# Kernel optimization log

Measured on AMD Instinct MI355X. Metric: run time of the kernel, lower is better.

Reference implementation:

```python
import jax, jax.numpy as jnp
import numpy as np

F_MAX = 16  # static max number of frames (torch code uses max(frames) dynamically)
B, C, H, W = 8, 5, 512, 512


def setup_inputs() -> dict:
    key = jax.random.key(0)
    k1, k2 = jax.random.split(key)
    inp = jax.random.normal(k1, (B, C, H, W), dtype=jnp.float32)
    frames = jax.random.randint(k2, (B,), 1, F_MAX + 1)  # n_frames per sample in [1, F_MAX]
    return {"input": inp, "frames": frames}


def _acquire(inp, frames, noise_key):
    b, _, h, w = inp.shape
    ku, kn = jax.random.split(noise_key)
    img = inp[:, :1]                                                   # [B,1,H,W]
    bias = jax.nn.relu(jnp.mean(inp[:, 1:2], axis=(1, 2, 3), keepdims=True))  # [B,1,1,1]
    sampled = img + bias                                               # broadcasts to [B,F_MAX,H,W] below
    center = img + bias                                                # [B,1,H,W]
    # Frechet noise
    fw = jax.nn.relu(inp[:, 2:3])                                      # weight [B,1,H,W]
    fa = jax.nn.relu(inp[:, 3:4])                                      # alpha  [B,1,H,W]
    u = jnp.clip(jax.random.uniform(ku, (b, F_MAX, h, w), dtype=inp.dtype), 1e-6, 1.0 - 1e-6)
    sampled = sampled + fw * (-jnp.log(u)) ** (-fa)                    # [B,F_MAX,H,W]
    center = center + fw * (1.0 / (fa + 1.0)) ** fa
    # Gaussian noise
    gw = jax.nn.relu(inp[:, 4:5])
    sampled = sampled + gw * jax.random.normal(kn, (b, F_MAX, h, w), dtype=inp.dtype)
    acquired_frames = jnp.clip(sampled, 0.0, 1.0)                      # [B,F_MAX,H,W]
    # ragged per-sample mean over first n_frames frames, vectorized via mask
    mask = (jnp.arange(F_MAX)[None, :, None, None] < frames[:, None, None, None]).astype(inp.dtype)
    frames_f = frames.astype(inp.dtype)[:, None, None, None]
    acquired = jnp.sum(acquired_frames * mask, axis=1, keepdims=True) / frames_f  # [B,1,H,W]
    return acquired, jnp.clip(center, 0.0, 1.0)


def reference(input, frames):
    return _acquire(input, frames, jax.random.key(42))
```

## Files before the change

kernel.cpp:

```cpp
#include <hip/hip_runtime.h>
#include <stdint.h>

#define HW 262144
#define ACQ_N 2097152
#define SREG 69632
#define NREG3 208896

#define CNT(b, c) ((((b) << 2) | (c)) << 5)

#define LOG2F(x) __builtin_amdgcn_logf(x)
#define EXP2F(x) __builtin_amdgcn_exp2f(x)
#define SQRTF(x) __builtin_amdgcn_sqrtf(x)
#define RCPF(x)  __builtin_amdgcn_rcpf(x)

#define ROTL(x, r) __builtin_amdgcn_alignbit((x), (x), (32 - (r)) & 31)

static inline void tf2x32_host(uint32_t k0, uint32_t k1, uint32_t c0, uint32_t c1,
                               uint32_t& o0, uint32_t& o1) {
  const uint32_t ks2 = k0 ^ k1 ^ 0x1BD11BDAu;
  uint32_t x0 = c0 + k0, x1 = c1 + k1;
#define TFR(r) { x0 += x1; x1 = (x1 << (r)) | (x1 >> (32 - (r))); x1 ^= x0; }
  TFR(13) TFR(15) TFR(26) TFR(6)
  x0 += k1;  x1 += ks2 + 1u;
  TFR(17) TFR(29) TFR(16) TFR(24)
  x0 += ks2; x1 += k0 + 2u;
  TFR(13) TFR(15) TFR(26) TFR(6)
  x0 += k0;  x1 += k1 + 3u;
  TFR(17) TFR(29) TFR(16) TFR(24)
  x0 += k1;  x1 += ks2 + 4u;
  TFR(13) TFR(15) TFR(26) TFR(6)
  x0 += ks2; x1 += k0 + 5u;
#undef TFR
  o0 = x0; o1 = x1;
}

__device__ __forceinline__ uint32_t rbits32(uint32_t k0, uint32_t k1, uint32_t idx) {
  const uint32_t ks2 = k0 ^ k1 ^ 0x1BD11BDAu;
  uint32_t x0 = k0, x1 = idx + k1;
#define TFR(r) { x0 += x1; x1 = ROTL(x1, r); x1 ^= x0; }
  TFR(13) TFR(15) TFR(26) TFR(6)
  x0 += k1;  x1 += ks2 + 1u;
  TFR(17) TFR(29) TFR(16) TFR(24)
  x0 += ks2; x1 += k0 + 2u;
  TFR(13) TFR(15) TFR(26) TFR(6)
  x0 += k0;  x1 += k1 + 3u;
  TFR(17) TFR(29) TFR(16) TFR(24)
  x0 += k1;  x1 += ks2 + 4u;
  TFR(13) TFR(15) TFR(26) TFR(6)
  x0 += ks2; x1 += k0 + 5u;
#undef TFR
  return x0 ^ x1;
}

__device__ __forceinline__ float unit_from_bits(uint32_t b) {
  return __uint_as_float((b >> 9) | 0x3F800000u) - 1.0f;
}

__device__ __forceinline__ float sqrt2_erfinv(float x) {
  float ome = fmaf(-x, x, 1.0f);
  float w = -0.69314718056f * LOG2F(ome);
  float wn = w - 2.5f;
  float p = 3.974065e-08f;
  p = fmaf(p, wn, 4.854641e-07f);
  p = fmaf(p, wn, -4.982823e-06f);
  p = fmaf(p, wn, -6.210531e-06f);
  p = fmaf(p, wn, 3.091200e-04f);
  p = fmaf(p, wn, -1.773035e-03f);
  p = fmaf(p, wn, -5.908135e-03f);
  p = fmaf(p, wn, 3.488029e-01f);
  p = fmaf(p, wn, 2.123314e+00f);
  if (__builtin_expect(w >= 5.0f, 0)) {
    float wf = SQRTF(w) - 3.0f;
    float q = -2.831458e-04f;
    q = fmaf(q, wf, 1.427657e-04f);
    q = fmaf(q, wf, 1.908260e-03f);
    q = fmaf(q, wf, -5.195013e-03f);
    q = fmaf(q, wf, 8.116892e-03f);
    q = fmaf(q, wf, -1.0779791e-02f);
    q = fmaf(q, wf, 1.3348579e-02f);
    q = fmaf(q, wf, 1.416582e+00f);
    q = fmaf(q, wf, 4.006434e+00f);
    p = q;
  }
  return p * x;
}

__device__ __forceinline__ float loop_fg(float base, float fw, float fa, float gw,
                                         uint32_t idx, int nf,
                                         uint32_t ku0, uint32_t ku1,
                                         uint32_t kn0, uint32_t kn1) {
  float nfa = -fa, fac = fa * 0.52876637294f;
  float acc = 0.0f;
#pragma unroll 2
  for (int f = 0; f < nf; ++f) {
    uint32_t ub = rbits32(ku0, ku1, idx);
    uint32_t nb = rbits32(kn0, kn1, idx);
    idx += (uint32_t)HW;
    float u = fminf(fmaxf(unit_from_bits(ub), 1e-6f), 0.999999f);
    float pw = EXP2F(fmaf(nfa, LOG2F(-LOG2F(u)), fac));
    float z = sqrt2_erfinv(fmaf(unit_from_bits(nb), 2.0f, -0.99999994f));
    float t = fmaf(gw, z, fmaf(fw, pw, base));
    acc += fminf(fmaxf(t, 0.0f), 1.0f);
  }
  return acc * RCPF((float)nf);
}

__device__ __forceinline__ float loop_f(float base, float fw, float fa,
                                        uint32_t idx, int nf,
                                        uint32_t ku0, uint32_t ku1) {
  float nfa = -fa, fac = fa * 0.52876637294f;
  float acc = 0.0f;
#pragma unroll 4
  for (int f = 0; f < nf; ++f) {
    uint32_t ub = rbits32(ku0, ku1, idx);
    idx += (uint32_t)HW;
    float u = fminf(fmaxf(unit_from_bits(ub), 1e-6f), 0.999999f);
    float pw = EXP2F(fmaf(nfa, LOG2F(-LOG2F(u)), fac));
    acc += fminf(fmaxf(fmaf(fw, pw, base), 0.0f), 1.0f);
  }
  return acc * RCPF((float)nf);
}

__device__ __forceinline__ float loop_g(float base, float gw,
                                        uint32_t idx, int nf,
                                        uint32_t kn0, uint32_t kn1) {
  float acc = 0.0f;
#pragma unroll 4
  for (int f = 0; f < nf; ++f) {
    uint32_t nb = rbits32(kn0, kn1, idx);
    idx += (uint32_t)HW;
    float z = sqrt2_erfinv(fmaf(unit_from_bits(nb), 2.0f, -0.99999994f));
    acc += fminf(fmaxf(fmaf(gw, z, base), 0.0f), 1.0f);
  }
  return acc * RCPF((float)nf);
}


__global__ __launch_bounds__(256) void bias_partial(const float* __restrict__ inp,
                                                    float* __restrict__ partial,
                                                    uint32_t* __restrict__ counters) {
  if (blockIdx.x == 0) {
    counters[threadIdx.x] = 0u;
    counters[256 + threadIdx.x] = 0u;
    counters[512 + threadIdx.x] = 0u;
    counters[768 + threadIdx.x] = 0u;
  }
  int blk = blockIdx.x;
  int b = blk >> 6, chunk = blk & 63;
  const float4* src = (const float4*)(inp + ((size_t)b * 5 + 1) * HW
                                          + (size_t)chunk * 4096);
  int t = threadIdx.x;
  float s = 0.0f;
#pragma unroll
  for (int k = 0; k < 4; ++k) {
    float4 v = src[t + k * 256];
    s += (v.x + v.y) + (v.z + v.w);
  }
  for (int off = 32; off; off >>= 1) s += __shfl_down(s, off);
  __shared__ float ws4[4];
  if ((t & 63) == 0) ws4[t >> 6] = s;
  __syncthreads();
  if (t == 0) partial[blk] = ws4[0] + ws4[1] + ws4[2] + ws4[3];
}

__global__ __launch_bounds__(256) void scatter_pack(const float* __restrict__ inp,
                                                    const float* __restrict__ partial,
                                                    uint32_t* __restrict__ counters,
                                                    uint32_t* __restrict__ remarr,
                                                    float4* __restrict__ packed,
                                                    float* __restrict__ out) {
  int blk = blockIdx.x;
  int b = blk >> 8, sub = blk & 255;
  int tid = threadIdx.x, lane = tid & 63, wid = tid >> 6;
  const float* pb = inp + (size_t)b * 5 * HW;
  uint64_t below = (1ull << lane) - 1ull;
  int base_i = sub << 10;

  __shared__ float s_bias;
  __shared__ uint32_t swcnt[4][4];
  __shared__ uint32_t sbase[4];

  if (tid < 64) {
    float s = partial[(b << 6) | tid];
    for (int o = 32; o; o >>= 1) s += __shfl_down(s, o);
    if (tid == 0) s_bias = fmaxf(s * (1.0f / 262144.0f), 0.0f);
  }

  float img4[4], fw4[4], fa4[4], gw4[4];
  uint32_t cls4[4];
  uint32_t wc1 = 0, wc2 = 0, wc3 = 0;
#pragma unroll
  for (int k = 0; k < 4; ++k) {
    int i = base_i + (k << 8) + tid;
    img4[k]  = pb[i];
    float f2 = pb[2 * HW + i];
    float f3 = pb[3 * HW + i];
    float f4 = pb[4 * HW + i];
    fw4[k] = fmaxf(f2, 0.0f);
    fa4[k] = fmaxf(f3, 0.0f);
    gw4[k] = fmaxf(f4, 0.0f);
    uint32_t cls = (f2 > 0.0f ? 1u : 0u) | (f4 > 0.0f ? 2u : 0u);
    cls4[k] = cls;
    wc1 += (uint32_t)__popcll(__ballot(cls == 1u));
    wc2 += (uint32_t)__popcll(__ballot(cls == 2u));
    wc3 += (uint32_t)__popcll(__ballot(cls == 3u));
  }
  if (lane == 0) {
    swcnt[wid][1] = wc1; swcnt[wid][2] = wc2; swcnt[wid][3] = wc3;
  }
  __syncthreads();
  if (tid < 3) {
    int c = tid + 1;
    uint32_t tot = swcnt[0][c] + swcnt[1][c] + swcnt[2][c] + swcnt[3][c];
    sbase[c] = atomicAdd(&counters[CNT(b, c)], tot);
  }
  __syncthreads();

  uint32_t run1 = sbase[1], run2 = sbase[2], run3 = sbase[3];
#pragma unroll
  for (int w = 0; w < 4; ++w) {
    if (w < wid) { run1 += swcnt[w][1]; run2 += swcnt[w][2]; run3 += swcnt[w][3]; }
  }
  float bias = s_bias;

  uint32_t* rbase = remarr + (size_t)b * NREG3;
  float4*   kbase = packed + (size_t)b * NREG3;
  float*    outa  = out + (size_t)b * HW;
  float*    outc  = out + ACQ_N + (size_t)b * HW;

#pragma unroll
  for (int k = 0; k < 4; ++k) {
    int i = base_i + (k << 8) + tid;
    float fw = fw4[k], fa = fa4[k], gw = gw4[k];
    float basev = img4[k] + bias;
    float cpw = EXP2F(-fa * LOG2F(fa + 1.0f));
    float ctr = fminf(fmaxf(fmaf(fw, cpw, basev), 0.0f), 1.0f);
    outc[i] = ctr;

    uint32_t cls = cls4[k];
    if (cls == 0u) outa[i] = ctr;

    uint64_t ba1 = __ballot(cls == 1u);
    uint64_t ba2 = __ballot(cls == 2u);
    uint64_t ba3 = __ballot(cls == 3u);
    if (cls != 0u) {
      uint64_t own  = (cls == 1u) ? ba1 : ((cls == 2u) ? ba2 : ba3);
      uint32_t rbas = (cls == 1u) ? run1 : ((cls == 2u) ? run2 : run3);
      uint32_t roff = (cls - 1u) * (uint32_t)SREG + rbas + (uint32_t)__popcll(own & below);
      rbase[roff] = (uint32_t)i;
      kbase[roff] = make_float4(basev, fw, fa, gw);
    }
    run1 += (uint32_t)__popcll(ba1);
    run2 += (uint32_t)__popcll(ba2);
    run3 += (uint32_t)__popcll(ba3);
  }
}

__global__ __launch_bounds__(256) void acquire_packed(
    const int* __restrict__ frames, const uint32_t* __restrict__ counters,
    const uint32_t* __restrict__ remarr, const float4* __restrict__ packed,
    float* __restrict__ out,
    uint32_t ku0, uint32_t ku1, uint32_t kn0, uint32_t kn1) {
  int c = 3 - (int)blockIdx.y;
  int b = (int)blockIdx.z;
  uint32_t cnt = counters[CNT(b, c)];
  uint32_t slot = ((uint32_t)blockIdx.x << 8) | (uint32_t)threadIdx.x;
  if (((uint32_t)blockIdx.x << 8) >= cnt) return;
  if (slot < cnt) {
    size_t roff = (size_t)b * NREG3 + (size_t)(c - 1) * SREG + slot;
    float4 op = packed[roff];
    uint32_t rem = remarr[roff];
    float base = op.x, fw = op.y, fa = op.z, gw = op.w;
    int nf = frames[b];
    uint32_t idx = ((uint32_t)b << 22) + rem;
    float res;
    if (c == 3)      res = loop_fg(base, fw, fa, gw, idx, nf, ku0, ku1, kn0, kn1);
    else if (c == 1) res = loop_f(base, fw, fa, idx, nf, ku0, ku1);
    else             res = loop_g(base, gw, idx, nf, kn0, kn1);
    out[(size_t)b * HW + rem] = res;
  }
}

__global__ __launch_bounds__(256) void bias_partial_plain(const float* __restrict__ inp,
                                                          float* __restrict__ partial) {
  int blk = blockIdx.x;
  int b = blk >> 6, chunk = blk & 63;
  const float4* src = (const float4*)(inp + ((size_t)b * 5 + 1) * HW
                                          + (size_t)chunk * 4096);
  int t = threadIdx.x;
  float s = 0.0f;
#pragma unroll
  for (int k = 0; k < 4; ++k) {
    float4 v = src[t + k * 256];
    s += (v.x + v.y) + (v.z + v.w);
  }
  for (int off = 32; off; off >>= 1) s += __shfl_down(s, off);
  __shared__ float ws4[4];
  if ((t & 63) == 0) ws4[t >> 6] = s;
  __syncthreads();
  if (t == 0) partial[blk] = ws4[0] + ws4[1] + ws4[2] + ws4[3];
}

__global__ __launch_bounds__(256) void acquire_plain(
    const float* __restrict__ inp, const int* __restrict__ frames,
    const float* __restrict__ partial, float* __restrict__ out,
    uint32_t ku0, uint32_t ku1, uint32_t kn0, uint32_t kn1) {
  int b = blockIdx.x >> 10;
  int rem = ((blockIdx.x & 1023) << 8) | threadIdx.x;
  __shared__ float s_bias;
  if (threadIdx.x < 64) {
    float s = partial[(b << 6) | threadIdx.x];
    for (int off = 32; off; off >>= 1) s += __shfl_down(s, off);
    if (threadIdx.x == 0) s_bias = fmaxf(s * (1.0f / 262144.0f), 0.0f);
  }
  const float* pb = inp + (size_t)b * 5 * HW;
  float img = pb[rem];
  float fw  = fmaxf(pb[2 * HW + rem], 0.0f);
  float fa  = fmaxf(pb[3 * HW + rem], 0.0f);
  float gw  = fmaxf(pb[4 * HW + rem], 0.0f);
  __syncthreads();
  float base = img + s_bias;
  int nf = frames[b];
  uint32_t idx = ((uint32_t)b << 22) + (uint32_t)rem;
  float res = loop_fg(base, fw, fa, gw, idx, nf, ku0, ku1, kn0, kn1);
  out[(size_t)b * HW + rem] = res;
  float cpw = EXP2F(-fa * LOG2F(fa + 1.0f));
  out[ACQ_N + (size_t)b * HW + rem] = fminf(fmaxf(fmaf(fw, cpw, base), 0.0f), 1.0f);
}

extern "C" void kernel_launch(void* const* d_in, const int* in_sizes, int n_in,
                              void* d_out, int out_size, void* d_ws, size_t ws_size,
                              hipStream_t stream) {
  const float* inp    = (const float*)d_in[0];
  const int*   frames = (const int*)d_in[1];
  float* out = (float*)d_out;

  uint32_t ku0, ku1, kn0, kn1;
  tf2x32_host(0u, 42u, 0u, 0u, ku0, ku1);
  tf2x32_host(0u, 42u, 0u, 1u, kn0, kn1);

  float*    partial  = (float*)d_ws;
  uint32_t* counters = (uint32_t*)((char*)d_ws + 4096);
  const size_t need_full = 8192 + (size_t)8 * NREG3 * 4 + (size_t)8 * NREG3 * 16;

  if (ws_size >= need_full) {
    uint32_t* remarr = (uint32_t*)((char*)d_ws + 8192);
    float4*   packed = (float4*)((char*)d_ws + 8192 + (size_t)8 * NREG3 * 4);
    bias_partial<<<dim3(512), dim3(256), 0, stream>>>(inp, partial, counters);
    scatter_pack<<<dim3(2048), dim3(256), 0, stream>>>(inp, partial, counters,
                                                       remarr, packed, out);
    acquire_packed<<<dim3(272, 3, 8), dim3(256), 0, stream>>>(frames, counters,
                                                              remarr, packed, out,
                                                              ku0, ku1, kn0, kn1);
  } else {
    bias_partial_plain<<<dim3(512), dim3(256), 0, stream>>>(inp, partial);
    acquire_plain<<<dim3(8192), dim3(256), 0, stream>>>(inp, frames, partial, out,
                                                        ku0, ku1, kn0, kn1);
  }
}
```

Before: 156.4 us.

## Split packed records per class and gather results via inverse map

Packed per-pixel records are split into one compact array per noise class, so the Gaussian-only class stores only gw and the index. The compute kernel re-reads the image value from the input instead of storing base, and writes its result in place into the packed slot. A new gather kernel reads an inverse map and writes results to the output in pixel order, replacing the scattered output writes. This aims to make output stores coalesced and shrink record traffic, at the cost of an extra kernel launch, a full-size inverse-map write and read, and a gathered image load in the compute kernel.

```diff
diff --git a/kernel.cpp b/kernel.cpp
--- a/kernel.cpp
+++ b/kernel.cpp
@@ -4,7 +4,6 @@
 #define HW 262144
 #define ACQ_N 2097152
 #define SREG 69632
-#define NREG3 208896
 
 #define CNT(b, c) ((((b) << 2) | (c)) << 5)
 
@@ -165,9 +164,12 @@
 
 __global__ __launch_bounds__(256) void scatter_pack(const float* __restrict__ inp,
                                                     const float* __restrict__ partial,
+                                                    float* __restrict__ biasv,
                                                     uint32_t* __restrict__ counters,
-                                                    uint32_t* __restrict__ remarr,
-                                                    float4* __restrict__ packed,
+                                                    float4* __restrict__ pk3,
+                                                    float4* __restrict__ pk1,
+                                                    float2* __restrict__ pk2,
+                                                    uint32_t* __restrict__ invmap,
                                                     float* __restrict__ out) {
   int blk = blockIdx.x;
   int b = blk >> 8, sub = blk & 255;
@@ -183,7 +185,11 @@
   if (tid < 64) {
     float s = partial[(b << 6) | tid];
     for (int o = 32; o; o >>= 1) s += __shfl_down(s, o);
-    if (tid == 0) s_bias = fmaxf(s * (1.0f / 262144.0f), 0.0f);
+    if (tid == 0) {
+      float bv = fmaxf(s * (1.0f / 262144.0f), 0.0f);
+      s_bias = bv;
+      if (sub == 0) biasv[b] = bv;
+    }
   }
 
   float img4[4], fw4[4], fa4[4], gw4[4];
@@ -223,8 +229,10 @@
   }
   float bias = s_bias;
 
-  uint32_t* rbase = remarr + (size_t)b * NREG3;
-  float4*   kbase = packed + (size_t)b * NREG3;
+  float4*   p3 = pk3 + (size_t)b * SREG;
+  float4*   p1 = pk1 + (size_t)b * SREG;
+  float2*   p2 = pk2 + (size_t)b * SREG;
+  uint32_t* im = invmap + (size_t)b * HW;
   float*    outa  = out + (size_t)b * HW;
   float*    outc  = out + ACQ_N + (size_t)b * HW;
 
@@ -238,18 +246,22 @@
     outc[i] = ctr;
 
     uint32_t cls = cls4[k];
-    if (cls == 0u) outa[i] = ctr;
-
     uint64_t ba1 = __ballot(cls == 1u);
     uint64_t ba2 = __ballot(cls == 2u);
     uint64_t ba3 = __ballot(cls == 3u);
-    if (cls != 0u) {
+    uint32_t imv = 0u;
+    if (cls == 0u) {
+      outa[i] = ctr;
+    } else {
       uint64_t own  = (cls == 1u) ? ba1 : ((cls == 2u) ? ba2 : ba3);
       uint32_t rbas = (cls == 1u) ? run1 : ((cls == 2u) ? run2 : run3);
-      uint32_t roff = (cls - 1u) * (uint32_t)SREG + rbas + (uint32_t)__popcll(own & below);
-      rbase[roff] = (uint32_t)i;
-      kbase[roff] = make_float4(basev, fw, fa, gw);
+      uint32_t slot = rbas + (uint32_t)__popcll(own & below);
+      imv = (cls << 28) | slot;
+      if (cls == 3u)      p3[slot] = make_float4(fw, fa, gw, __uint_as_float((uint32_t)i));
+      else if (cls == 1u) p1[slot] = make_float4(fw, fa, __uint_as_float((uint32_t)i), 0.0f);
+      else                p2[slot] = make_float2(gw, __uint_as_float((uint32_t)i));
     }
+    im[i] = imv;
     run1 += (uint32_t)__popcll(ba1);
     run2 += (uint32_t)__popcll(ba2);
     run3 += (uint32_t)__popcll(ba3);
@@ -257,9 +269,9 @@
 }
 
 __global__ __launch_bounds__(256) void acquire_packed(
-    const int* __restrict__ frames, const uint32_t* __restrict__ counters,
-    const uint32_t* __restrict__ remarr, const float4* __restrict__ packed,
-    float* __restrict__ out,
+    const float* __restrict__ inp, const int* __restrict__ frames,
+    const float* __restrict__ biasv, const uint32_t* __restrict__ counters,
+    float4* __restrict__ pk3, float4* __restrict__ pk1, float2* __restrict__ pk2,
     uint32_t ku0, uint32_t ku1, uint32_t kn0, uint32_t kn1) {
   int c = 3 - (int)blockIdx.y;
   int b = (int)blockIdx.z;
@@ -267,17 +279,49 @@
   uint32_t slot = ((uint32_t)blockIdx.x << 8) | (uint32_t)threadIdx.x;
   if (((uint32_t)blockIdx.x << 8) >= cnt) return;
   if (slot < cnt) {
-    size_t roff = (size_t)b * NREG3 + (size_t)(c - 1) * SREG + slot;
-    float4 op = packed[roff];
-    uint32_t rem = remarr[roff];
-    float base = op.x, fw = op.y, fa = op.z, gw = op.w;
+    size_t rb = (size_t)b * SREG + slot;
     int nf = frames[b];
-    uint32_t idx = ((uint32_t)b << 22) + rem;
+    float bias = biasv[b];
+    const float* pimg = inp + (size_t)b * 5 * HW;
     float res;
-    if (c == 3)      res = loop_fg(base, fw, fa, gw, idx, nf, ku0, ku1, kn0, kn1);
-    else if (c == 1) res = loop_f(base, fw, fa, idx, nf, ku0, ku1);
-    else             res = loop_g(base, gw, idx, nf, kn0, kn1);
-    out[(size_t)b * HW + rem] = res;
+    if (c == 3) {
+      float4 v = pk3[rb];
+      uint32_t rem = __float_as_uint(v.w);
+      float base = pimg[rem] + bias;
+      res = loop_fg(base, v.x, v.y, v.z, ((uint32_t)b << 22) + rem, nf,
+                    ku0, ku1, kn0, kn1);
+      ((float*)pk3)[rb * 4] = res;
+    } else if (c == 1) {
+      float4 v = pk1[rb];
+      uint32_t rem = __float_as_uint(v.z);
+      float base = pimg[rem] + bias;
+      res = loop_f(base, v.x, v.y, ((uint32_t)b << 22) + rem, nf, ku0, ku1);
+      ((float*)pk1)[rb * 4] = res;
+    } else {
+      float2 v = pk2[rb];
+      uint32_t rem = __float_as_uint(v.y);
+      float base = pimg[rem] + bias;
+      res = loop_g(base, v.x, ((uint32_t)b << 22) + rem, nf, kn0, kn1);
+      ((float*)pk2)[rb * 2] = res;
+    }
+  }
+}
+
+__global__ __launch_bounds__(256) void gather_out(
+    const uint32_t* __restrict__ invmap,
+    const float4* __restrict__ pk3, const float4* __restrict__ pk1,
+    const float2* __restrict__ pk2, float* __restrict__ out) {
+  int b = blockIdx.x >> 10;
+  int i = ((blockIdx.x & 1023) << 8) | threadIdx.x;
+  uint32_t im = invmap[(size_t)b * HW + i];
+  if (im) {
+    uint32_t cls = im >> 28;
+    size_t rb = (size_t)b * SREG + (im & 0x0FFFFFFFu);
+    float res;
+    if (cls == 3u)      res = ((const float*)pk3)[rb * 4];
+    else if (cls == 1u) res = ((const float*)pk1)[rb * 4];
+    else                res = ((const float*)pk2)[rb * 2];
+    out[(size_t)b * HW + i] = res;
   }
 }
 
@@ -340,18 +384,31 @@
   tf2x32_host(0u, 42u, 0u, 1u, kn0, kn1);
 
   float*    partial  = (float*)d_ws;
+  float*    biasv    = (float*)((char*)d_ws + 2048);
   uint32_t* counters = (uint32_t*)((char*)d_ws + 4096);
-  const size_t need_full = 8192 + (size_t)8 * NREG3 * 4 + (size_t)8 * NREG3 * 16;
+
+  const size_t PK3_OFF = 16384;
+  const size_t PK3_B   = (size_t)8 * SREG * 16;
+  const size_t PK1_OFF = PK3_OFF + PK3_B;
+  const size_t PK1_B   = (size_t)8 * SREG * 16;
+  const size_t PK2_OFF = PK1_OFF + PK1_B;
+  const size_t PK2_B   = (size_t)8 * SREG * 8;
+  const size_t IM_OFF  = PK2_OFF + PK2_B;
+  const size_t IM_B    = (size_t)8 * HW * 4;
+  const size_t need_full = IM_OFF + IM_B;
 
   if (ws_size >= need_full) {
-    uint32_t* remarr = (uint32_t*)((char*)d_ws + 8192);
-    float4*   packed = (float4*)((char*)d_ws + 8192 + (size_t)8 * NREG3 * 4);
+    float4*   pk3    = (float4*)((char*)d_ws + PK3_OFF);
+    float4*   pk1    = (float4*)((char*)d_ws + PK1_OFF);
+    float2*   pk2    = (float2*)((char*)d_ws + PK2_OFF);
+    uint32_t* invmap = (uint32_t*)((char*)d_ws + IM_OFF);
     bias_partial<<<dim3(512), dim3(256), 0, stream>>>(inp, partial, counters);
-    scatter_pack<<<dim3(2048), dim3(256), 0, stream>>>(inp, partial, counters,
-                                                       remarr, packed, out);
-    acquire_packed<<<dim3(272, 3, 8), dim3(256), 0, stream>>>(frames, counters,
-                                                              remarr, packed, out,
+    scatter_pack<<<dim3(2048), dim3(256), 0, stream>>>(inp, partial, biasv, counters,
+                                                       pk3, pk1, pk2, invmap, out);
+    acquire_packed<<<dim3(272, 3, 8), dim3(256), 0, stream>>>(inp, frames, biasv,
+                                                              counters, pk3, pk1, pk2,
                                                               ku0, ku1, kn0, kn1);
+    gather_out<<<dim3(8192), dim3(256), 0, stream>>>(invmap, pk3, pk1, pk2, out);
   } else {
     bias_partial_plain<<<dim3(512), dim3(256), 0, stream>>>(inp, partial);
     acquire_plain<<<dim3(8192), dim3(256), 0, stream>>>(inp, frames, partial, out,
```

Measured after the change: 166.5 us. 6.4% more time.
